# Kernel tuning notes

Measured on AMD Instinct MI355X. Metric: run time of the kernel, lower is better.

Reference implementation:

```python
import jax, jax.numpy as jnp
import numpy as np

HIDDEN = 2048
NUM_HEADS = 32
NUM_KV_HEADS = 8
HEAD_DIM = 128
EPS = 1e-6
ROPE_BASE = 10000.0
T = 2048


def setup_inputs() -> dict:
    key = jax.random.key(0)
    k1, k2, k3, k4, k5 = jax.random.split(key, 5)
    q_size = NUM_HEADS * HEAD_DIM
    kv_size = NUM_KV_HEADS * HEAD_DIM
    s = 0.02
    return {
        "positions": jnp.arange(T, dtype=jnp.int32),
        "hidden_states": jax.random.normal(k1, (T, HIDDEN), dtype=jnp.float32),
        "wqkv": jax.random.normal(k2, (q_size + 2 * kv_size, HIDDEN), dtype=jnp.float32) * s,
        "wo": jax.random.normal(k3, (HIDDEN, q_size), dtype=jnp.float32) * s,
        "q_norm_w": jnp.ones((HEAD_DIM,), dtype=jnp.float32),
        "k_norm_w": jnp.ones((HEAD_DIM,), dtype=jnp.float32),
    }


def _rms_norm(x, w, eps=EPS):
    # x: [T, H, D]; normalize over last dim
    var = jnp.mean(jnp.square(x), axis=-1, keepdims=True)
    return x * jax.lax.rsqrt(var + eps) * w


def _rope(positions, x):
    # neox-style rotate-half RoPE. x: [T, H, D]
    half = HEAD_DIM // 2
    inv_freq = 1.0 / (ROPE_BASE ** (jnp.arange(0, half, dtype=jnp.float32) / half))
    ang = positions.astype(jnp.float32)[:, None] * inv_freq  # [T, half]
    cos = jnp.cos(ang)[:, None, :]  # [T, 1, half]
    sin = jnp.sin(ang)[:, None, :]
    x1, x2 = x[..., :half], x[..., half:]
    return jnp.concatenate([x1 * cos - x2 * sin, x2 * cos + x1 * sin], axis=-1)


def reference(positions, hidden_states, wqkv, wo, q_norm_w, k_norm_w):
    q_size = NUM_HEADS * HEAD_DIM
    kv_size = NUM_KV_HEADS * HEAD_DIM
    scaling = HEAD_DIM ** -0.5

    qkv = hidden_states @ wqkv.T  # [T, q_size + 2*kv_size]
    q = qkv[:, :q_size].reshape(-1, NUM_HEADS, HEAD_DIM)
    k = qkv[:, q_size:q_size + kv_size].reshape(-1, NUM_KV_HEADS, HEAD_DIM)
    v = qkv[:, q_size + kv_size:].reshape(-1, NUM_KV_HEADS, HEAD_DIM)

    q = _rms_norm(q, q_norm_w)
    k = _rms_norm(k, k_norm_w)
    q = _rope(positions, q)
    k = _rope(positions, k)

    # GQA: repeat kv heads to match query heads
    group = NUM_HEADS // NUM_KV_HEADS
    k = jnp.repeat(k, group, axis=1)  # [T, H, D]
    v = jnp.repeat(v, group, axis=1)

    scores = jnp.einsum("thd,shd->hts", q, k) * scaling  # [H, T, T]
    causal = positions[:, None] >= positions[None, :]  # [T, T]
    scores = jnp.where(causal[None], scores, jnp.finfo(scores.dtype).min)
    probs = jax.nn.softmax(scores, axis=-1)
    o = jnp.einsum("hts,shd->thd", probs, v)  # [T, H, D]
    return o.reshape(-1, q_size) @ wo.T  # [T, HIDDEN]
```

## Files before the change

### kernel.cpp

```cpp
#include <hip/hip_runtime.h>
#include <hip/hip_bf16.h>

#define T_SEQ   2048
#define HIDDEN  2048
#define NUM_H   32
#define NUM_KV  8
#define HD      128
#define Q_SIZE  4096
#define QKV_N   6144

typedef __bf16 bf16;
typedef __bf16 bf16x8 __attribute__((ext_vector_type(8)));
typedef __bf16 bf16x4 __attribute__((ext_vector_type(4)));
typedef float  floatx4 __attribute__((ext_vector_type(4)));

#define GLOBAL_AS(p) ((const __attribute__((address_space(1))) void*)(p))
#define LDS_AS(p)    ((__attribute__((address_space(3))) void*)(p))

__global__ void detect_dtype(const unsigned short* __restrict__ wq, int* flagp)
{
    const int lane = threadIdx.x;
    int cnt = 0;
    for (int i = lane; i < 512; i += 64) {
        int ef = (wq[i] >> 7) & 0xFF;
        if (ef >= 90 && ef <= 130) cnt++;
    }
    #pragma unroll
    for (int m = 32; m; m >>= 1) cnt += __shfl_xor(cnt, m);
    if (lane == 0) *flagp = (cnt >= 430) ? 1 : 0;
}

__global__ __launch_bounds__(256) void convert_all(
    const void* __restrict__ h, const void* __restrict__ wq,
    const void* __restrict__ wo_, const void* __restrict__ qn,
    const void* __restrict__ kn,
    bf16* __restrict__ hb, bf16* __restrict__ wqb, bf16* __restrict__ wob,
    bf16* __restrict__ qnb, bf16* __restrict__ knb, const int* flagp)
{
    long e = ((long)blockIdx.x * 256 + threadIdx.x) * 8;
    const void* src; bf16* dst; long off;
    if      (e < 4194304)  { src = h;   dst = hb;  off = e; }
    else if (e < 16777216) { src = wq;  dst = wqb; off = e - 4194304; }
    else if (e < 25165824) { src = wo_; dst = wob; off = e - 16777216; }
    else if (e < 25165952) { src = qn;  dst = qnb; off = e - 25165824; }
    else if (e < 25166080) { src = kn;  dst = knb; off = e - 25165952; }
    else return;

    if (*flagp) {
        *(bf16x8*)(dst + off) = *(const bf16x8*)((const bf16*)src + off);
    } else {
        const float* f = (const float*)src + off;
        bf16x8 v;
        #pragma unroll
        for (int i = 0; i < 8; ++i) v[i] = (bf16)f[i];
        *(bf16x8*)(dst + off) = v;
    }
}

__global__ __launch_bounds__(256) void gemm_bt(
    const bf16* __restrict__ A, const bf16* __restrict__ B,
    void* __restrict__ Cv, int M, int N, int K, int lda,
    const int* flagp, int is_final)
{
    __shared__ bf16 As[128 * 32];
    __shared__ bf16 Bs[128 * 32];

    const int tid  = threadIdx.x;
    const int wave = tid >> 6, lane = tid & 63;
    const int quad = lane >> 4, l16 = lane & 15;
    const int wm = (wave & 1) * 64, wn = (wave >> 1) * 64;
    const long baseM = (long)blockIdx.x * 128;
    const long baseN = (long)blockIdx.y * 128;
    const int  bf_out = is_final ? *flagp : 1;

    const int  srow = wave * 16 + (lane >> 2);
    const int  scol = (lane & 3) * 8;
    const long aoff0 = (baseM + srow) * (long)lda + scol;
    const long aoff1 = (baseM + 64 + srow) * (long)lda + scol;
    const long boff0 = (baseN + srow) * (long)K + scol;
    const long boff1 = (baseN + 64 + srow) * (long)K + scol;
    const int  lds0 = wave * 512;
    const int  lds1 = 2048 + wave * 512;

    floatx4 acc[4][4] = {};

    for (int k0 = 0; k0 < K; k0 += 32) {
        __builtin_amdgcn_global_load_lds(GLOBAL_AS(A + aoff0 + k0), LDS_AS(As + lds0), 16, 0, 0);
        __builtin_amdgcn_global_load_lds(GLOBAL_AS(A + aoff1 + k0), LDS_AS(As + lds1), 16, 0, 0);
        __builtin_amdgcn_global_load_lds(GLOBAL_AS(B + boff0 + k0), LDS_AS(Bs + lds0), 16, 0, 0);
        __builtin_amdgcn_global_load_lds(GLOBAL_AS(B + boff1 + k0), LDS_AS(Bs + lds1), 16, 0, 0);
        __syncthreads();

        bf16x8 af[4], bfr[4];
        #pragma unroll
        for (int i = 0; i < 4; ++i)
            af[i] = *(const bf16x8*)(As + (wm + i * 16 + l16) * 32 + quad * 8);
        #pragma unroll
        for (int j = 0; j < 4; ++j)
            bfr[j] = *(const bf16x8*)(Bs + (wn + j * 16 + l16) * 32 + quad * 8);

        #pragma unroll
        for (int i = 0; i < 4; ++i)
            #pragma unroll
            for (int j = 0; j < 4; ++j)
                acc[i][j] = __builtin_amdgcn_mfma_f32_16x16x32_bf16(af[i], bfr[j], acc[i][j], 0, 0, 0);
        __syncthreads();
    }

    #pragma unroll
    for (int i = 0; i < 4; ++i)
        #pragma unroll
        for (int j = 0; j < 4; ++j)
            #pragma unroll
            for (int r = 0; r < 4; ++r) {
                long row = baseM + wm + i * 16 + quad * 4 + r;
                long col = baseN + wn + j * 16 + l16;
                if (bf_out) ((bf16*)Cv)[row * (long)N + col] = (bf16)acc[i][j][r];
                else       ((float*)Cv)[row * (long)N + col] = acc[i][j][r];
            }
}

__global__ __launch_bounds__(256) void gemm_db(
    const bf16* __restrict__ A, const bf16* __restrict__ B,
    float* __restrict__ Cp, int N, int Kd, int lda, int ldb)
{
    __shared__ bf16 As[2][128 * 32];
    __shared__ bf16 Bs[2][128 * 32];

    const int tid  = threadIdx.x;
    const int wave = tid >> 6, lane = tid & 63;
    const int quad = lane >> 4, l16 = lane & 15;
    const int wm = (wave & 1) * 64, wn = (wave >> 1) * 64;
    const long baseM = (long)blockIdx.x * 128;
    const long baseN = (long)blockIdx.y * 128;
    const long koff  = (long)blockIdx.z * Kd;

    const int  srow = wave * 16 + (lane >> 2);
    const int  scol = (lane & 3) * 8;
    const long aoff0 = (baseM + srow) * (long)lda + koff + scol;
    const long aoff1 = (baseM + 64 + srow) * (long)lda + koff + scol;
    const long boff0 = (baseN + srow) * (long)ldb + koff + scol;
    const long boff1 = (baseN + 64 + srow) * (long)ldb + koff + scol;
    const int  lds0 = wave * 512;
    const int  lds1 = 2048 + wave * 512;

    auto stage = [&](int p, int k0) {
        __builtin_amdgcn_global_load_lds(GLOBAL_AS(A + aoff0 + k0), LDS_AS(As[p] + lds0), 16, 0, 0);
        __builtin_amdgcn_global_load_lds(GLOBAL_AS(A + aoff1 + k0), LDS_AS(As[p] + lds1), 16, 0, 0);
        __builtin_amdgcn_global_load_lds(GLOBAL_AS(B + boff0 + k0), LDS_AS(Bs[p] + lds0), 16, 0, 0);
        __builtin_amdgcn_global_load_lds(GLOBAL_AS(B + boff1 + k0), LDS_AS(Bs[p] + lds1), 16, 0, 0);
    };

    floatx4 acc[4][4] = {};

    stage(0, 0);
    asm volatile("s_waitcnt vmcnt(0)" ::: "memory");
    __builtin_amdgcn_s_barrier();

    int cur = 0;
    for (int k0 = 0; k0 < Kd; k0 += 32) {
        if (k0 + 32 < Kd) stage(cur ^ 1, k0 + 32);
        __builtin_amdgcn_sched_barrier(0);

        bf16x8 af[4], bfr[4];
        #pragma unroll
        for (int i = 0; i < 4; ++i)
            af[i] = *(const bf16x8*)(As[cur] + (wm + i * 16 + l16) * 32 + quad * 8);
        #pragma unroll
        for (int j = 0; j < 4; ++j)
            bfr[j] = *(const bf16x8*)(Bs[cur] + (wn + j * 16 + l16) * 32 + quad * 8);

        #pragma unroll
        for (int i = 0; i < 4; ++i)
            #pragma unroll
            for (int j = 0; j < 4; ++j)
                acc[i][j] = __builtin_amdgcn_mfma_f32_16x16x32_bf16(af[i], bfr[j], acc[i][j], 0, 0, 0);

        asm volatile("s_waitcnt vmcnt(0)" ::: "memory");
        __builtin_amdgcn_s_barrier();
        cur ^= 1;
    }

    const long Mrows = (long)gridDim.x * 128;
    float* C = Cp + (long)blockIdx.z * Mrows * N;
    #pragma unroll
    for (int i = 0; i < 4; ++i)
        #pragma unroll
        for (int j = 0; j < 4; ++j)
            #pragma unroll
            for (int r = 0; r < 4; ++r) {
                long row = baseM + wm + i * 16 + quad * 4 + r;
                long col = baseN + wn + j * 16 + l16;
                C[row * (long)N + col] = acc[i][j][r];
            }
}

__global__ __launch_bounds__(256) void reduce2(
    const float* __restrict__ P0, const float* __restrict__ P1,
    void* __restrict__ out, const int* flagp)
{
    long i = ((long)blockIdx.x * 256 + threadIdx.x) * 4;
    floatx4 a = *(const floatx4*)(P0 + i);
    floatx4 b = *(const floatx4*)(P1 + i);
    floatx4 s = a + b;
    if (*flagp) {
        bf16x4 o;
        #pragma unroll
        for (int r = 0; r < 4; ++r) o[r] = (bf16)s[r];
        *(bf16x4*)((bf16*)out + i) = o;
    } else {
        *(floatx4*)((float*)out + i) = s;
    }
}

__global__ __launch_bounds__(256) void qkv_post(
    bf16* __restrict__ qkv, const int* __restrict__ positions,
    const bf16* __restrict__ qnw, const bf16* __restrict__ knw)
{
    const int t = blockIdx.x;
    const int tid = threadIdx.x, wave = tid >> 6, lane = tid & 63;
    const float pos = (float)positions[t];

    const float inv = expf(-(float)lane * (float)(9.210340371976184 / 64.0));
    float sn, cs;
    sincosf(pos * inv, &sn, &cs);

    bf16* row = qkv + (long)t * QKV_N;

    for (int u = wave; u < 40; u += 4) {
        bf16* p       = (u < 32) ? row + u * HD : row + Q_SIZE + (u - 32) * HD;
        const bf16* w = (u < 32) ? qnw : knw;
        float x1 = (float)p[lane], x2 = (float)p[lane + 64];
        float ss = x1 * x1 + x2 * x2;
        #pragma unroll
        for (int m = 32; m; m >>= 1) ss += __shfl_xor(ss, m);
        float rr = rsqrtf(ss * (1.f / 128.f) + 1e-6f);
        float y1 = x1 * rr * (float)w[lane];
        float y2 = x2 * rr * (float)w[lane + 64];
        p[lane]      = (bf16)(y1 * cs - y2 * sn);
        p[lane + 64] = (bf16)(y2 * cs + y1 * sn);
    }
}

__global__ __launch_bounds__(256) void vtrans(const bf16* __restrict__ qkv,
                                              bf16* __restrict__ vt)
{
    __shared__ bf16 tile[64][136];
    const int t0 = blockIdx.x * 64, kvh = blockIdx.y, tid = threadIdx.x;

    const int rl = tid >> 4, c8 = (tid & 15) * 8;
    const bf16* src = qkv + (long)t0 * QKV_N + 5120 + kvh * HD;
    #pragma unroll
    for (int it = 0; it < 4; ++it) {
        int r = it * 16 + rl;
        *(bf16x8*)(&tile[r][c8]) = *(const bf16x8*)(src + (long)r * QKV_N + c8);
    }
    __syncthreads();

    const int d = tid >> 1, tb = (tid & 1) * 32;
    bf16* dst = vt + ((long)kvh * HD + d) * T_SEQ + t0 + tb;
    #pragma unroll
    for (int it = 0; it < 4; ++it) {
        bf16x8 v;
        #pragma unroll
        for (int j = 0; j < 8; ++j) v[j] = tile[tb + it * 8 + j][d];
        *(bf16x8*)(dst + it * 8) = v;
    }
}

__global__ __launch_bounds__(256, 3) void attn5(bf16* qkv, const bf16* __restrict__ vt)
{
    __shared__ bf16 Ks[2][64 * 128];
    __shared__ bf16 Vs[128 * 64];

    const int tid  = threadIdx.x, wave = tid >> 6, lane = tid & 63;
    const int quad = lane >> 4, l16 = lane & 15;
    const int h = blockIdx.x, kvh = h >> 2;
    const int iq = 31 - blockIdx.y;
    const int q0 = iq * 64;

    const float C1 = 0.12753236f;
    const float C2 = 17.312340f;

    bf16x8 qf[4];
    {
        const bf16* qa = qkv + (long)(q0 + wave * 16 + l16) * QKV_N + h * HD + quad * 8;
        #pragma unroll
        for (int ks = 0; ks < 4; ++ks) qf[ks] = *(const bf16x8*)(qa + ks * 32);
    }

    floatx4 oacc[8] = {};
    float ls = 0.f;

    const int krl = lane >> 4, kc = lane & 15;
    const int vrl = lane >> 3, vc = lane & 7;
    const int kswz = (kc ^ (wave * 4 + krl)) * 8;
    const int vswz = (vc ^ (vrl & 7)) * 8;
    const int wsig = ((wave & 1) << 1) | (wave >> 1);
    const int sq4  = (((quad & 1) << 1) | (quad >> 1)) << 2;

    const bf16* kg0 = qkv + Q_SIZE + kvh * HD;
    const bf16* vg0 = vt + (long)kvh * HD * T_SEQ;

    auto stageK = [&](int p, int kt) {
        const bf16* kg = kg0 + (long)(kt * 64) * QKV_N;
        #pragma unroll
        for (int it = 0; it < 4; ++it) {
            const int rK = it * 16 + wsig * 4 + krl;
            __builtin_amdgcn_global_load_lds(GLOBAL_AS(kg + (long)rK * QKV_N + kswz),
                                             LDS_AS(&Ks[p][it * 2048 + wave * 512]), 16, 0, 0);
        }
    };
    auto stageV = [&](int kt) {
        const bf16* vg = vg0 + kt * 64;
        #pragma unroll
        for (int it = 0; it < 4; ++it) {
            const int dV = it * 32 + wave * 8 + vrl;
            __builtin_amdgcn_global_load_lds(GLOBAL_AS(vg + (long)dV * T_SEQ + vswz),
                                             LDS_AS(&Vs[it * 2048 + wave * 512]), 16, 0, 0);
        }
    };

    stageK(0, 0);

    const int qg = q0 + wave * 16 + l16;

    for (int kt = 0; kt <= iq; ++kt) {
        const int p = kt & 1;
        __syncthreads();
        stageV(kt);
        if (kt < iq) stageK(p ^ 1, kt + 1);

        const int k0 = kt * 64;

        floatx4 sT[4] = {};
        #pragma unroll
        for (int j2 = 0; j2 < 4; ++j2)
            #pragma unroll
            for (int ks = 0; ks < 4; ++ks) {
                bf16x8 kf = *(const bf16x8*)(&Ks[p][(j2 * 16 + l16) * 128 + (((ks * 4 + quad) ^ l16) * 8)]);
                sT[j2] = __builtin_amdgcn_mfma_f32_16x16x32_bf16(kf, qf[ks], sT[j2], 0, 0, 0);
            }

        const bool diag = (kt == iq);
        unsigned lov[4], hiv[4];
        #pragma unroll
        for (int j2 = 0; j2 < 4; ++j2) {
            float ev[4];
            #pragma unroll
            for (int r = 0; r < 4; ++r) {
                float x = __builtin_amdgcn_exp2f(sT[j2][r] * C1 - C2);
                if (diag && (k0 + j2 * 16 + sq4 + r > qg)) x = 0.f;
                ls += x;
                ev[r] = x;
            }
            asm("v_cvt_pk_bf16_f32 %0, %1, %2" : "=v"(lov[j2]) : "v"(ev[0]), "v"(ev[1]));
            asm("v_cvt_pk_bf16_f32 %0, %1, %2" : "=v"(hiv[j2]) : "v"(ev[2]), "v"(ev[3]));
        }

        bf16x8 pa[2];
        #pragma unroll
        for (int ks2 = 0; ks2 < 2; ++ks2) {
            auto wl = __builtin_amdgcn_permlane32_swap(lov[2 * ks2], lov[2 * ks2 + 1], false, false);
            auto wh = __builtin_amdgcn_permlane32_swap(hiv[2 * ks2], hiv[2 * ks2 + 1], false, false);
            union { unsigned w[4]; bf16x8 v; } u;
            u.w[0] = wl[0]; u.w[1] = wh[0]; u.w[2] = wl[1]; u.w[3] = wh[1];
            pa[ks2] = u.v;
        }

        if (kt < iq) asm volatile("s_waitcnt vmcnt(4)" ::: "memory");
        else         asm volatile("s_waitcnt vmcnt(0)" ::: "memory");
        __builtin_amdgcn_s_barrier();
        __builtin_amdgcn_sched_barrier(0);

        #pragma unroll
        for (int ks2 = 0; ks2 < 2; ++ks2)
            #pragma unroll
            for (int vj = 0; vj < 8; ++vj) {
                const int d = vj * 16 + l16;
                bf16x8 vb = *(const bf16x8*)(&Vs[d * 64 + (((ks2 * 4 + quad) ^ (d & 7)) * 8)]);
                oacc[vj] = __builtin_amdgcn_mfma_f32_16x16x32_bf16(pa[ks2], vb, oacc[vj], 0, 0, 0);
            }
    }

    ls += __shfl_xor(ls, 16); ls += __shfl_xor(ls, 32);
    float rinv[4];
    #pragma unroll
    for (int r = 0; r < 4; ++r) rinv[r] = 1.f / __shfl(ls, quad * 4 + r);

    #pragma unroll
    for (int vj = 0; vj < 8; ++vj)
        #pragma unroll
        for (int r = 0; r < 4; ++r) {
            const long row = q0 + wave * 16 + quad * 4 + r;
            qkv[row * (long)QKV_N + h * HD + vj * 16 + l16] = (bf16)(oacc[vj][r] * rinv[r]);
        }
}

extern "C" void kernel_launch(void* const* d_in, const int* in_sizes, int n_in,
                              void* d_out, int out_size, void* d_ws, size_t ws_size,
                              hipStream_t stream)
{
    const int* positions = (const int*)d_in[0];

    char* ws = (char*)d_ws;
    bf16* qkv  = (bf16*)(ws);
    bf16* hb   = (bf16*)(ws + 25165824);
    bf16* vt   = hb;
    float* P0  = (float*)(ws + 25165824);
    float* P1  = (float*)(ws + 41943040);
    bf16* wqb  = (bf16*)(ws + 33554432);
    bf16* wob  = (bf16*)(ws + 58720256);
    bf16* qnb  = (bf16*)(ws + 75497472);
    bf16* knb  = (bf16*)(ws + 75497728);
    int*  flag = (int*) (ws + 75497984);

    detect_dtype<<<dim3(1), dim3(64), 0, stream>>>((const unsigned short*)d_in[2], flag);
    convert_all<<<dim3(12289), dim3(256), 0, stream>>>(
        d_in[1], d_in[2], d_in[3], d_in[4], d_in[5],
        hb, wqb, wob, qnb, knb, flag);

    dim3 blk(256);
    gemm_bt<<<dim3(T_SEQ / 128, QKV_N / 128), blk, 0, stream>>>(
        hb, wqb, qkv, T_SEQ, QKV_N, HIDDEN, HIDDEN, flag, 0);
    vtrans<<<dim3(T_SEQ / 64, NUM_KV), blk, 0, stream>>>(qkv, vt);
    qkv_post<<<dim3(T_SEQ), blk, 0, stream>>>(qkv, positions, qnb, knb);
    attn5<<<dim3(NUM_H, 32), blk, 0, stream>>>(qkv, vt);
    gemm_db<<<dim3(T_SEQ / 128, HIDDEN / 128, 2), blk, 0, stream>>>(
        qkv, wob, P0, HIDDEN, Q_SIZE / 2, QKV_N, Q_SIZE);
    reduce2<<<dim3(4096), blk, 0, stream>>>(P0, P1, d_out, flag);
}
```

Before: 342.3 us.

## Replace QKV projection GEMM with 256x256 double-buffered swizzled 8-wave kernel

Replaces the single-buffered 128x128 QKV projection GEMM with a 512-thread kernel that computes 256x256 tiles. It uses K=64 chunks, double-buffered LDS staging via global_load_lds, and an XOR-swizzled LDS layout to avoid bank conflicts. The next tile's loads overlap with MFMA work through a partial vmcnt wait, and s_setprio raises wave priority around the MFMA bursts. The aim is more data reuse per tile and hidden load latency. In exchange, the kernel uses 128KB of LDS and more accumulator registers, and the grid drops to 192 blocks, which may underfill the CUs.

New measurement: 329.6 us. 3.7% less time.

```diff
diff --git a/kernel.cpp b/kernel.cpp
--- a/kernel.cpp
+++ b/kernel.cpp
@@ -16,6 +16,10 @@
 
 #define GLOBAL_AS(p) ((const __attribute__((address_space(1))) void*)(p))
 #define LDS_AS(p)    ((__attribute__((address_space(3))) void*)(p))
+
+#define BARRIER() do { asm volatile("" ::: "memory"); \
+                       __builtin_amdgcn_s_barrier();  \
+                       asm volatile("" ::: "memory"); } while (0)
 
 __global__ void detect_dtype(const unsigned short* __restrict__ wq, int* flagp)
 {
@@ -57,66 +61,144 @@
     }
 }
 
-__global__ __launch_bounds__(256) void gemm_bt(
+__global__ __launch_bounds__(512, 2) void gemm8p(
     const bf16* __restrict__ A, const bf16* __restrict__ B,
-    void* __restrict__ Cv, int M, int N, int K, int lda,
-    const int* flagp, int is_final)
-{
-    __shared__ bf16 As[128 * 32];
-    __shared__ bf16 Bs[128 * 32];
+    bf16* __restrict__ C, int N, int K, int lda, int ldb)
+{
+    __shared__ bf16 As[2][2][128 * 64];
+    __shared__ bf16 Bs[2][2][128 * 64];
 
     const int tid  = threadIdx.x;
     const int wave = tid >> 6, lane = tid & 63;
     const int quad = lane >> 4, l16 = lane & 15;
-    const int wm = (wave & 1) * 64, wn = (wave >> 1) * 64;
-    const long baseM = (long)blockIdx.x * 128;
-    const long baseN = (long)blockIdx.y * 128;
-    const int  bf_out = is_final ? *flagp : 1;
-
-    const int  srow = wave * 16 + (lane >> 2);
-    const int  scol = (lane & 3) * 8;
-    const long aoff0 = (baseM + srow) * (long)lda + scol;
-    const long aoff1 = (baseM + 64 + srow) * (long)lda + scol;
-    const long boff0 = (baseN + srow) * (long)K + scol;
-    const long boff1 = (baseN + 64 + srow) * (long)K + scol;
-    const int  lds0 = wave * 512;
-    const int  lds1 = 2048 + wave * 512;
-
-    floatx4 acc[4][4] = {};
-
-    for (int k0 = 0; k0 < K; k0 += 32) {
-        __builtin_amdgcn_global_load_lds(GLOBAL_AS(A + aoff0 + k0), LDS_AS(As + lds0), 16, 0, 0);
-        __builtin_amdgcn_global_load_lds(GLOBAL_AS(A + aoff1 + k0), LDS_AS(As + lds1), 16, 0, 0);
-        __builtin_amdgcn_global_load_lds(GLOBAL_AS(B + boff0 + k0), LDS_AS(Bs + lds0), 16, 0, 0);
-        __builtin_amdgcn_global_load_lds(GLOBAL_AS(B + boff1 + k0), LDS_AS(Bs + lds1), 16, 0, 0);
-        __syncthreads();
-
-        bf16x8 af[4], bfr[4];
-        #pragma unroll
-        for (int i = 0; i < 4; ++i)
-            af[i] = *(const bf16x8*)(As + (wm + i * 16 + l16) * 32 + quad * 8);
+    const int wm = wave >> 2;
+    const int wn = wave & 3;
+    const int wh = wn >> 1;
+    const int bro = (wn & 1) * 64;
+    const long baseM = (long)blockIdx.x * 256;
+    const long baseN = (long)blockIdx.y * 256;
+
+    auto stage = [&](int p, int t) {
+        const long kc = (long)t * 64;
+        #pragma unroll
+        for (int l = 0; l < 8; ++l) {
+            const int h   = (l >> 1) & 1;
+            const int n0  = (l & 1) * 512 + wave * 64;
+            const int n   = n0 + lane;
+            const int row = n >> 3, slot = n & 7;
+            const int gc  = (slot ^ (row & 7)) * 8;
+            if (l < 4)
+                __builtin_amdgcn_global_load_lds(
+                    GLOBAL_AS(A + (baseM + h * 128 + row) * (long)lda + kc + gc),
+                    LDS_AS(&As[p][h][n0 * 8]), 16, 0, 0);
+            else
+                __builtin_amdgcn_global_load_lds(
+                    GLOBAL_AS(B + (baseN + h * 128 + row) * (long)ldb + kc + gc),
+                    LDS_AS(&Bs[p][h][n0 * 8]), 16, 0, 0);
+        }
+    };
+
+    floatx4 acc[8][4] = {};
+
+    stage(0, 0);
+
+    const int NT = K / 64;
+    for (int t = 0; t < NT; ++t) {
+        const int p = t & 1;
+        if (t + 1 < NT) {
+            stage(p ^ 1, t + 1);
+            asm volatile("s_waitcnt vmcnt(8)" ::: "memory");
+        } else {
+            asm volatile("s_waitcnt vmcnt(0)" ::: "memory");
+        }
+        __builtin_amdgcn_sched_barrier(0);
+        BARRIER();
+
+        const bf16* Aw = &As[p][wm][0];
+        const bf16* Bw = &Bs[p][wh][0];
+
+        bf16x8 af[4][2], bf0[2][2], bf1[2][2];
+
+        #pragma unroll
+        for (int mf = 0; mf < 4; ++mf)
+            #pragma unroll
+            for (int ks = 0; ks < 2; ++ks) {
+                const int r = mf * 16 + l16;
+                af[mf][ks] = *(const bf16x8*)(Aw + r * 64 + (((ks * 4 + quad) ^ (r & 7)) * 8));
+            }
+        #pragma unroll
+        for (int nf = 0; nf < 2; ++nf)
+            #pragma unroll
+            for (int ks = 0; ks < 2; ++ks) {
+                const int r = bro + nf * 16 + l16;
+                bf0[nf][ks] = *(const bf16x8*)(Bw + r * 64 + (((ks * 4 + quad) ^ (r & 7)) * 8));
+            }
+        __builtin_amdgcn_s_setprio(1);
+        #pragma unroll
+        for (int mf = 0; mf < 4; ++mf)
+            #pragma unroll
+            for (int nf = 0; nf < 2; ++nf)
+                #pragma unroll
+                for (int ks = 0; ks < 2; ++ks)
+                    acc[mf][nf] = __builtin_amdgcn_mfma_f32_16x16x32_bf16(af[mf][ks], bf0[nf][ks], acc[mf][nf], 0, 0, 0);
+        __builtin_amdgcn_s_setprio(0);
+
+        #pragma unroll
+        for (int nf = 0; nf < 2; ++nf)
+            #pragma unroll
+            for (int ks = 0; ks < 2; ++ks) {
+                const int r = bro + (nf + 2) * 16 + l16;
+                bf1[nf][ks] = *(const bf16x8*)(Bw + r * 64 + (((ks * 4 + quad) ^ (r & 7)) * 8));
+            }
+        __builtin_amdgcn_s_setprio(1);
+        #pragma unroll
+        for (int mf = 0; mf < 4; ++mf)
+            #pragma unroll
+            for (int nf = 0; nf < 2; ++nf)
+                #pragma unroll
+                for (int ks = 0; ks < 2; ++ks)
+                    acc[mf][nf + 2] = __builtin_amdgcn_mfma_f32_16x16x32_bf16(af[mf][ks], bf1[nf][ks], acc[mf][nf + 2], 0, 0, 0);
+        __builtin_amdgcn_s_setprio(0);
+
+        #pragma unroll
+        for (int mf = 0; mf < 4; ++mf)
+            #pragma unroll
+            for (int ks = 0; ks < 2; ++ks) {
+                const int r = (mf + 4) * 16 + l16;
+                af[mf][ks] = *(const bf16x8*)(Aw + r * 64 + (((ks * 4 + quad) ^ (r & 7)) * 8));
+            }
+        __builtin_amdgcn_s_setprio(1);
+        #pragma unroll
+        for (int mf = 0; mf < 4; ++mf)
+            #pragma unroll
+            for (int nf = 0; nf < 2; ++nf)
+                #pragma unroll
+                for (int ks = 0; ks < 2; ++ks)
+                    acc[mf + 4][nf] = __builtin_amdgcn_mfma_f32_16x16x32_bf16(af[mf][ks], bf0[nf][ks], acc[mf + 4][nf], 0, 0, 0);
+        __builtin_amdgcn_s_setprio(0);
+
+        __builtin_amdgcn_s_setprio(1);
+        #pragma unroll
+        for (int mf = 0; mf < 4; ++mf)
+            #pragma unroll
+            for (int nf = 0; nf < 2; ++nf)
+                #pragma unroll
+                for (int ks = 0; ks < 2; ++ks)
+                    acc[mf + 4][nf + 2] = __builtin_amdgcn_mfma_f32_16x16x32_bf16(af[mf][ks], bf1[nf][ks], acc[mf + 4][nf + 2], 0, 0, 0);
+        __builtin_amdgcn_s_setprio(0);
+
+        BARRIER();
+    }
+
+    #pragma unroll
+    for (int i = 0; i < 8; ++i)
         #pragma unroll
         for (int j = 0; j < 4; ++j)
-            bfr[j] = *(const bf16x8*)(Bs + (wn + j * 16 + l16) * 32 + quad * 8);
-
-        #pragma unroll
-        for (int i = 0; i < 4; ++i)
-            #pragma unroll
-            for (int j = 0; j < 4; ++j)
-                acc[i][j] = __builtin_amdgcn_mfma_f32_16x16x32_bf16(af[i], bfr[j], acc[i][j], 0, 0, 0);
-        __syncthreads();
-    }
-
-    #pragma unroll
-    for (int i = 0; i < 4; ++i)
-        #pragma unroll
-        for (int j = 0; j < 4; ++j)
             #pragma unroll
             for (int r = 0; r < 4; ++r) {
-                long row = baseM + wm + i * 16 + quad * 4 + r;
-                long col = baseN + wn + j * 16 + l16;
-                if (bf_out) ((bf16*)Cv)[row * (long)N + col] = (bf16)acc[i][j][r];
-                else       ((float*)Cv)[row * (long)N + col] = acc[i][j][r];
+                long row = baseM + wm * 128 + i * 16 + quad * 4 + r;
+                long col = baseN + wn * 64 + j * 16 + l16;
+                C[row * (long)N + col] = (bf16)acc[i][j][r];
             }
 }
 
@@ -420,13 +502,12 @@
         d_in[1], d_in[2], d_in[3], d_in[4], d_in[5],
         hb, wqb, wob, qnb, knb, flag);
 
-    dim3 blk(256);
-    gemm_bt<<<dim3(T_SEQ / 128, QKV_N / 128), blk, 0, stream>>>(
-        hb, wqb, qkv, T_SEQ, QKV_N, HIDDEN, HIDDEN, flag, 0);
-    vtrans<<<dim3(T_SEQ / 64, NUM_KV), blk, 0, stream>>>(qkv, vt);
-    qkv_post<<<dim3(T_SEQ), blk, 0, stream>>>(qkv, positions, qnb, knb);
-    attn5<<<dim3(NUM_H, 32), blk, 0, stream>>>(qkv, vt);
-    gemm_db<<<dim3(T_SEQ / 128, HIDDEN / 128, 2), blk, 0, stream>>>(
+    gemm8p<<<dim3(T_SEQ / 256, QKV_N / 256), dim3(512), 0, stream>>>(
+        hb, wqb, qkv, QKV_N, HIDDEN, HIDDEN, HIDDEN);
+    vtrans<<<dim3(T_SEQ / 64, NUM_KV), dim3(256), 0, stream>>>(qkv, vt);
+    qkv_post<<<dim3(T_SEQ), dim3(256), 0, stream>>>(qkv, positions, qnb, knb);
+    attn5<<<dim3(NUM_H, 32), dim3(256), 0, stream>>>(qkv, vt);
+    gemm_db<<<dim3(T_SEQ / 128, HIDDEN / 128, 2), dim3(256), 0, stream>>>(
         qkv, wob, P0, HIDDEN, Q_SIZE / 2, QKV_N, Q_SIZE);
-    reduce2<<<dim3(4096), blk, 0, stream>>>(P0, P1, d_out, flag);
-}
+    reduce2<<<dim3(4096), dim3(256), 0, stream>>>(P0, P1, d_out, flag);
+}
```
